# Kernel tuning notes

Hardware: AMD Instinct MI355X
Metric: run time of the kernel (lower is better)

Reference implementation:

```python
import jax, jax.numpy as jnp
import numpy as np

B, T, HID = 4, 4096, 768
H, D = 12, 64
N_HASHES = 2
BUCKET_SIZE = T // 32          # reformer repo config: max_seq_len // 32 = 128
N_BUCKETS = T // BUCKET_SIZE   # 32
SELF_ATTN_VALUE = -5e4         # reformer_pytorch TOKEN_SELF_ATTN_VALUE
MASK_VALUE = -1e9


def lsh_attention(X, mask_bool, W_qk, W_v, rotations):
    # X: [b, t, hid]; rotations: [d, n_hashes, n_buckets//2] (shared across batch & heads)
    b, t, _ = X.shape
    d, n_hashes, half_nb = rotations.shape
    n_buckets = 2 * half_nb
    h = W_qk.shape[0] // d
    scale = d ** -0.5

    qk = X @ W_qk.T            # shared query/key projection (bias-free in reformer_pytorch)
    v = X @ W_v.T

    def merge_heads(x):  # [b,t,h*d] -> [b*h, t, d]
        return x.reshape(b, t, h, d).transpose(0, 2, 1, 3).reshape(b * h, t, d)

    qk, v = merge_heads(qk), merge_heads(v)
    maskbh = jnp.repeat(mask_bool, h, axis=0)          # [bh, t]

    # --- LSH bucketing ---
    rotated = jnp.einsum('btf,fhi->bhti', qk, rotations)          # [bh, nh, t, nb/2]
    rotated = jnp.concatenate([rotated, -rotated], axis=-1)       # [bh, nh, t, nb]
    buckets = jnp.argmax(rotated, axis=-1)                        # [bh, nh, t]
    offsets = (jnp.arange(n_hashes) * n_buckets)[None, :, None]
    buckets = (buckets + offsets).reshape(b * h, n_hashes * t)

    # --- stable sort by (bucket, position) ---
    total = n_hashes * t
    ticker = jnp.arange(total)[None, :]
    buckets_and_t = buckets * t + (ticker % t)
    sticker = jnp.argsort(buckets_and_t, axis=-1)   # stable
    undo = jnp.argsort(sticker, axis=-1)
    st = sticker % t                                 # original positions, sorted order

    sqk = jnp.take_along_axis(qk, st[..., None], axis=1)
    sv = jnp.take_along_axis(v, st[..., None], axis=1)
    smask = jnp.take_along_axis(maskbh, st, axis=1)

    # --- chunk; each chunk attends to itself + previous chunk ---
    n_chunks = n_hashes * n_buckets
    cl = total // n_chunks                                  # == bucket_size
    bq_t = st.reshape(b * h, n_chunks, cl)
    bqk = sqk.reshape(b * h, n_chunks, cl, d)
    bv = sv.reshape(b * h, n_chunks, cl, d)
    bmask = smask.reshape(b * h, n_chunks, cl)

    bq = bqk
    bk = bqk / jnp.clip(jnp.linalg.norm(bqk, axis=-1, keepdims=True), 1e-12)

    def look_one_back(x):
        return jnp.concatenate([x, jnp.roll(x, 1, axis=1)], axis=2)

    bk, bv = look_one_back(bk), look_one_back(bv)
    bkv_t = look_one_back(bq_t)
    bkv_mask = look_one_back(bmask)

    dots = jnp.einsum('bnie,bnje->bnij', bq, bk) * scale    # [bh, n_chunks, cl, 2cl]
    pad = bmask[..., :, None] & bkv_mask[..., None, :]
    dots = jnp.where(pad, dots, MASK_VALUE)
    self_mask = bq_t[..., :, None] == bkv_t[..., None, :]
    dots = jnp.where(self_mask, SELF_ATTN_VALUE, dots)

    lse = jax.scipy.special.logsumexp(dots, axis=-1, keepdims=True)
    probs = jnp.exp(dots - lse)
    bo = jnp.einsum('bnij,bnje->bnie', probs, bv)

    # --- unsort and combine hash rounds via softmax over round logsumexps ---
    so = bo.reshape(b * h, total, d)
    slogits = lse.reshape(b * h, total)
    o = jnp.take_along_axis(so, undo[..., None], axis=1)
    logits = jnp.take_along_axis(slogits, undo, axis=1)

    o = o.reshape(b * h, n_hashes, t, d)
    logits = logits.reshape(b * h, n_hashes, t, 1)
    round_probs = jnp.exp(logits - jax.scipy.special.logsumexp(logits, axis=1, keepdims=True))
    out = jnp.sum(o * round_probs, axis=1)                  # [bh, t, d]
    return out.reshape(b, h, t, d).transpose(0, 2, 1, 3).reshape(b, t, h * d)


def setup_inputs() -> dict:
    key = jax.random.key(0)
    ks = jax.random.split(key, 8)
    s = 1.0 / np.sqrt(HID)
    return {
        'X': jax.random.normal(ks[0], (B, T, HID), jnp.float32),
        'mask': jnp.ones((B, T), jnp.float32),
        'W_qk': jax.random.uniform(ks[1], (H * D, HID), jnp.float32, -s, s),
        'W_v': jax.random.uniform(ks[2], (H * D, HID), jnp.float32, -s, s),
        'rotations': jax.random.normal(ks[3], (D, N_HASHES, N_BUCKETS // 2), jnp.float32),
        'W_to': jax.random.uniform(ks[4], (HID, H * D), jnp.float32, -s, s),
        'b_to': jnp.zeros((HID,), jnp.float32),
        'W_o': jax.random.uniform(ks[5], (HID, HID), jnp.float32, -s, s),
        'b_o': jnp.zeros((HID,), jnp.float32),
    }


def reference(X, mask, W_qk, W_v, rotations, W_to, b_to, W_o, b_o):
    attn = lsh_attention(X, mask.astype(bool), W_qk, W_v, rotations)
    attn = attn @ W_to.T + b_to     # LSHSelfAttention.to_out
    return attn @ W_o.T + b_o       # ReformerAttention.W_o
```

## Files before the change

kernel.cpp:

```cpp
#include <hip/hip_runtime.h>
#include <hip/hip_bf16.h>
#include <math.h>


typedef __attribute__((ext_vector_type(8))) short bf16x8;
typedef __attribute__((ext_vector_type(4))) float f32x4;
typedef __attribute__((ext_vector_type(4))) double f64x4;

__device__ __forceinline__ float bf_lo(unsigned int w) { return __uint_as_float(w << 16); }
__device__ __forceinline__ float bf_hi(unsigned int w) { return __uint_as_float(w & 0xffff0000u); }
__device__ __forceinline__ float load_in(const void* p, size_t i, bool f32) {
  return f32 ? ((const float*)p)[i]
             : __bfloat162float(((const __hip_bfloat16*)p)[i]);
}
__device__ __forceinline__ unsigned short f2bf(float x) {
  __hip_bfloat16 h = __float2bfloat16(x);
  return *reinterpret_cast<unsigned short*>(&h);
}
__device__ __forceinline__ float bf2f(unsigned short u) { return __uint_as_float(((unsigned int)u) << 16); }

__global__ void k_detect(const unsigned int* __restrict__ X, int* __restrict__ flag) {
  if (threadIdx.x == 0 && blockIdx.x == 0) {
    int vote = 0;
    for (int i = 0; i < 64; ++i) {
      unsigned int e = (X[i] >> 7) & 0xffu;
      vote += (e >= 100u && e <= 141u) ? 1 : 0;
    }
    *flag = (vote < 32) ? 1 : 0;
  }
}

__global__ __launch_bounds__(256) void k_convert(
    const void* __restrict__ src, unsigned short* __restrict__ dst, int n8,
    const int* __restrict__ flag) {
  const bool f32in = (*flag != 0);
  int i = blockIdx.x * 256 + threadIdx.x;
  if (i >= n8) return;
  if (f32in) {
    const float4* s = (const float4*)src + (size_t)i * 2;
    float4 a = s[0], b = s[1];
    union { unsigned short u[8]; uint4 v; } o;
    o.u[0] = f2bf(a.x); o.u[1] = f2bf(a.y); o.u[2] = f2bf(a.z); o.u[3] = f2bf(a.w);
    o.u[4] = f2bf(b.x); o.u[5] = f2bf(b.y); o.u[6] = f2bf(b.z); o.u[7] = f2bf(b.w);
    ((uint4*)dst)[i] = o.v;
  } else {
    ((uint4*)dst)[i] = ((const uint4*)src)[i];
  }
}

__global__ __launch_bounds__(256) void k_build_wrot(
    const void* __restrict__ Wqk, const void* __restrict__ rot,
    double* __restrict__ WrotT, const int* __restrict__ flag) {
  const bool f32in = (*flag != 0);
  int idx = blockIdx.x * 256 + threadIdx.x;
  if (idx >= 768 * 384) return;
  int row = idx % 384;
  int c   = idx / 384;
  int hh = row >> 5, hi = row & 31;
  double s = 0.0;
  for (int f = 0; f < 64; ++f) {
    double rv = (double)load_in(rot, f * 32 + hi, f32in);
    double wv = (double)load_in(Wqk, (size_t)(hh * 64 + f) * 768 + c, f32in);
    s = fma(rv, wv, s);
  }
  WrotT[(size_t)c * 384 + row] = s;
}

__global__ __launch_bounds__(512) void k_bucket(
    const void* __restrict__ X, const double* __restrict__ WrotT,
    unsigned char* __restrict__ cls, const int* __restrict__ flag) {
  const bool f32in = (*flag != 0);
  __shared__ double SH[4224];
  float* XsF = (float*)SH;
  double* Sc = SH;
  const int tid = threadIdx.x;
  const int M0 = blockIdx.x * 128;
  const int N0 = blockIdx.y * 64;
  const int w = tid >> 6, lane = tid & 63;
  const int l15 = lane & 15, lq = lane >> 4;
  const int sr = tid >> 2, sh2 = tid & 3;
  const int wk = tid >> 5, wg2 = (tid & 31) * 2;

  f64x4 acc[4];
  #pragma unroll
  for (int j = 0; j < 4; ++j) acc[j] = (f64x4){0.0, 0.0, 0.0, 0.0};

  int rowid[4], colid[4];
  {
    f64x4 zz = (f64x4){0.0, 0.0, 0.0, 0.0};
    f64x4 pr = __builtin_amdgcn_mfma_f64_16x16x4f64(
        (double)l15, (lq == 0) ? 1.0 : 0.0, zz, 0, 0, 0);
    f64x4 pc = __builtin_amdgcn_mfma_f64_16x16x4f64(
        (lq == 0) ? 1.0 : 0.0, (double)l15, zz, 0, 0, 0);
    #pragma unroll
    for (int r = 0; r < 4; ++r) {
      rowid[r] = (int)pr[r];
      colid[r] = (int)pc[r];
    }
  }

  float xv[4];
  double wvv[2];
  auto load_chunk = [&](int k0) {
    size_t base = (size_t)(M0 + sr) * 768 + k0 + sh2 * 4;
    if (f32in) {
      float4 f0 = *(const float4*)((const float*)X + base);
      xv[0] = f0.x; xv[1] = f0.y; xv[2] = f0.z; xv[3] = f0.w;
    } else {
      uint2 u = *(const uint2*)((const unsigned short*)X + base);
      xv[0] = bf_lo(u.x); xv[1] = bf_hi(u.x);
      xv[2] = bf_lo(u.y); xv[3] = bf_hi(u.y);
    }
    const double* wp = WrotT + (size_t)(k0 + wk) * 384 + N0 + wg2;
    wvv[0] = wp[0]; wvv[1] = wp[1];
  };
  auto store_stage = [&](int bsel) {
    float* Xs = XsF + bsel * 2112;
    double* Ws = SH + 2112 + bsel * 1056;
    #pragma unroll
    for (int j = 0; j < 4; ++j) Xs[(sh2 * 4 + j) * 132 + sr] = xv[j];
    Ws[wk * 66 + wg2] = wvv[0];
    Ws[wk * 66 + wg2 + 1] = wvv[1];
  };

  load_chunk(0);
  store_stage(0);
  __syncthreads();
  for (int t = 0; t < 48; ++t) {
    const float* Xs = XsF + (t & 1) * 2112;
    const double* Ws = SH + 2112 + (t & 1) * 1056;
    if (t < 47) load_chunk((t + 1) * 16);
    #pragma unroll
    for (int kq = 0; kq < 4; ++kq) {
      double a = (double)Xs[(kq * 4 + lq) * 132 + w * 16 + l15];
      const double* wr = &Ws[(kq * 4 + lq) * 66 + l15];
      #pragma unroll
      for (int nt = 0; nt < 4; ++nt)
        acc[nt] = __builtin_amdgcn_mfma_f64_16x16x4f64(a, wr[nt * 16], acc[nt], 0, 0, 0);
    }
    if (t < 47) store_stage((t & 1) ^ 1);
    __syncthreads();
  }

  #pragma unroll
  for (int chunk = 0; chunk < 2; ++chunk) {
    __syncthreads();
    if ((w >> 2) == chunk) {
      int lr = (w & 3) * 16;
      #pragma unroll
      for (int nt = 0; nt < 4; ++nt)
        #pragma unroll
        for (int r = 0; r < 4; ++r)
          Sc[(nt * 16 + colid[r]) * 66 + lr + rowid[r]] = acc[nt][r];
    }
    __syncthreads();
    for (int task = tid; task < 256; task += 512) {
      int g = task >> 6, tok = task & 63;
      const double* s = &Sc[(g * 16) * 66 + tok];
      double mx = -1.0e300;
      #pragma unroll
      for (int i = 0; i < 16; ++i) {
        double a = s[i * 66];
        mx = fmax(mx, fmax(a, -a));
      }
      int amax = 0;
      #pragma unroll
      for (int i = 15; i >= 0; --i) if (-s[i * 66] == mx) amax = 16 + i;
      #pragma unroll
      for (int i = 15; i >= 0; --i) if (s[i * 66] == mx) amax = i;
      int m = M0 + chunk * 64 + tok;
      int b = m >> 12, t = m & 4095;
      int gg = blockIdx.y * 4 + g, hh = gg >> 1, h = gg & 1;
      cls[(size_t)(b * 12 + hh) * 8192 + h * 4096 + t] = (unsigned char)(h * 32 + amax);
    }
  }
}

__global__ __launch_bounds__(1024) void k_sort(
    const unsigned char* __restrict__ clsg,
    unsigned short* __restrict__ stick) {
  __shared__ unsigned short cntg[128 * 64];
  __shared__ int classbase[64];
  const int row = blockIdx.x;
  const int tid = threadIdx.x;
  const int wave = tid >> 6, lane = tid & 63;
  const unsigned char* cr = clsg + ((size_t)row << 13);

  for (int i = tid; i < 128 * 64 / 2; i += 1024) ((uint32_t*)cntg)[i] = 0;
  __syncthreads();

  unsigned char myc[8], myrank[8];
  const unsigned long long ltmask = (lane == 0) ? 0ull : (~0ull >> (64 - lane));
  #pragma unroll
  for (int chunk = 0; chunk < 8; ++chunk) {
    int g = chunk * 16 + wave;
    int j = g * 64 + lane;
    int c = cr[j];
    unsigned long long same = ~0ull;
    #pragma unroll
    for (int bit = 0; bit < 6; ++bit) {
      unsigned long long bm = __ballot((c >> bit) & 1);
      same &= ((c >> bit) & 1) ? bm : ~bm;
    }
    int rank = __popcll(same & ltmask);
    if (rank == 0) cntg[g * 64 + c] = (unsigned short)__popcll(same);
    myc[chunk] = (unsigned char)c;
    myrank[chunk] = (unsigned char)rank;
  }
  __syncthreads();
  if (tid < 64) {
    int run = 0;
    for (int g = 0; g < 128; ++g) {
      int t = cntg[g * 64 + tid];
      cntg[g * 64 + tid] = (unsigned short)run;
      run += t;
    }
    classbase[tid] = run;
  }
  __syncthreads();
  if (tid == 0) {
    int run = 0;
    for (int c = 0; c < 64; ++c) { int t = classbase[c]; classbase[c] = run; run += t; }
  }
  __syncthreads();
  unsigned short* out = stick + ((size_t)row << 13);
  #pragma unroll
  for (int chunk = 0; chunk < 8; ++chunk) {
    int g = chunk * 16 + wave;
    int j = g * 64 + lane;
    int c = myc[chunk];
    int pos = classbase[c] + cntg[g * 64 + c] + myrank[chunk];
    out[pos] = (unsigned short)j;
  }
}

__global__ __launch_bounds__(256) void k_gemm_mfma(
    const unsigned short* __restrict__ A, const unsigned short* __restrict__ W,
    const void* __restrict__ bias, void* __restrict__ Cout,
    int layout, int out_ext, const int* __restrict__ flag) {
  const bool f32in = (*flag != 0);
  const bool oF32 = out_ext && f32in;
  __shared__ unsigned short As[128 * 40];
  __shared__ unsigned short Bs[128 * 40];
  const int tid = threadIdx.x;
  const int bm = blockIdx.x, bn = blockIdx.y;
  const int w = tid >> 6, lane = tid & 63;
  const int l15 = lane & 15, lq = lane >> 4;
  const int wm = (w >> 1) * 64, wn = (w & 1) * 64;
  const int r4 = tid >> 2, c4 = tid & 3;
  const unsigned short* Ag = A + (size_t)(bm * 128 + r4) * 768 + c4 * 8;
  const unsigned short* Bg = W + (size_t)(bn * 128 + r4) * 768 + c4 * 8;
  f32x4 acc[4][4];
  #pragma unroll
  for (int i = 0; i < 4; ++i)
    #pragma unroll
    for (int j = 0; j < 4; ++j) acc[i][j] = (f32x4){0.f, 0.f, 0.f, 0.f};
  uint4 pa0 = *(const uint4*)(Ag);
  uint4 pa1 = *(const uint4*)(Ag + 64 * 768);
  uint4 pb0 = *(const uint4*)(Bg);
  uint4 pb1 = *(const uint4*)(Bg + 64 * 768);
  for (int kt = 0; kt < 24; ++kt) {
    __syncthreads();
    *(uint4*)&As[r4 * 40 + c4 * 8] = pa0;
    *(uint4*)&As[(r4 + 64) * 40 + c4 * 8] = pa1;
    *(uint4*)&Bs[r4 * 40 + c4 * 8] = pb0;
    *(uint4*)&Bs[(r4 + 64) * 40 + c4 * 8] = pb1;
    __syncthreads();
    if (kt < 23) {
      int off = (kt + 1) * 32;
      pa0 = *(const uint4*)(Ag + off);
      pa1 = *(const uint4*)(Ag + 64 * 768 + off);
      pb0 = *(const uint4*)(Bg + off);
      pb1 = *(const uint4*)(Bg + 64 * 768 + off);
    }
    bf16x8 af[4], bfr[4];
    #pragma unroll
    for (int mt = 0; mt < 4; ++mt)
      af[mt] = *(const bf16x8*)&As[(wm + mt * 16 + l15) * 40 + lq * 8];
    #pragma unroll
    for (int nt = 0; nt < 4; ++nt)
      bfr[nt] = *(const bf16x8*)&Bs[(wn + nt * 16 + l15) * 40 + lq * 8];
    #pragma unroll
    for (int mt = 0; mt < 4; ++mt)
      #pragma unroll
      for (int nt = 0; nt < 4; ++nt)
        acc[mt][nt] = __builtin_amdgcn_mfma_f32_16x16x32_bf16(af[mt], bfr[nt], acc[mt][nt], 0, 0, 0);
  }
  #pragma unroll
  for (int mt = 0; mt < 4; ++mt) {
    #pragma unroll
    for (int nt = 0; nt < 4; ++nt) {
      #pragma unroll
      for (int reg = 0; reg < 4; ++reg) {
        int m = bm * 128 + wm + mt * 16 + lq * 4 + reg;
        int n = bn * 128 + wn + nt * 16 + l15;
        float val = acc[mt][nt][reg];
        if (bias != nullptr) val += load_in(bias, n, f32in);
        if (layout == 0) {
          size_t addr = (size_t)m * 768 + n;
          if (oF32) ((float*)Cout)[addr] = val;
          else      ((unsigned short*)Cout)[addr] = f2bf(val);
        } else {
          int b2 = m >> 12, t2 = m & 4095, hh = n >> 6, f = n & 63;
          ((unsigned short*)Cout)[((((size_t)(b2 * 12 + hh)) << 12) + t2) * 64 + f] = f2bf(val);
        }
      }
    }
  }
}

__global__ __launch_bounds__(256) void k_norm(
    const unsigned short* __restrict__ qk, float* __restrict__ nk) {
  int row = blockIdx.x * 32 + (threadIdx.x >> 3);
  int cs = threadIdx.x & 7;
  const uint4* p = (const uint4*)(qk + (size_t)row * 64);
  uint4 wv = p[cs];
  float s = 0.f;
  float e;
  e = bf_lo(wv.x); s += e * e;  e = bf_hi(wv.x); s += e * e;
  e = bf_lo(wv.y); s += e * e;  e = bf_hi(wv.y); s += e * e;
  e = bf_lo(wv.z); s += e * e;  e = bf_hi(wv.z); s += e * e;
  e = bf_lo(wv.w); s += e * e;  e = bf_hi(wv.w); s += e * e;
  s += __shfl_xor(s, 1, 64);
  s += __shfl_xor(s, 2, 64);
  s += __shfl_xor(s, 4, 64);
  if (cs == 0) nk[row] = 1.0f / fmaxf(sqrtf(s), 1e-12f);
}

__global__ __launch_bounds__(256) void k_attn_mfma(
    const unsigned short* __restrict__ qk,
    const unsigned short* __restrict__ vv,
    const unsigned short* __restrict__ stick,
    const void* __restrict__ mask,
    const float* __restrict__ nk,
    unsigned short* __restrict__ o_r,
    float* __restrict__ lse_r,
    const int* __restrict__ flag) {
  const bool f32in = (*flag != 0);
  __shared__ unsigned short Qs[128 * 72];
  __shared__ unsigned short Ks[64 * 72];
  __shared__ unsigned short Vt[64 * 72];
  __shared__ unsigned short Ps[4 * 32 * 72];
  __shared__ unsigned short Tq[128];
  __shared__ unsigned short Tkv[64];
  __shared__ float Nkv[64];
  unsigned short* Vs = Ps;

  const int tid = threadIdx.x;
  const int bh = blockIdx.x >> 6;
  const int ci = blockIdx.x & 63;
  const int b  = bh / 12;
  const int prev = (ci + 63) & 63;
  const int w = tid >> 6, lane = tid & 63;
  const int l15 = lane & 15, lq = lane >> 4;
  const unsigned short* srow = stick + ((size_t)bh << 13);
  const int jrow = tid >> 3, cs = tid & 7;

  #pragma unroll
  for (int pass = 0; pass < 4; ++pass) {
    int r = jrow + pass * 32;
    int s = srow[ci * 128 + r];
    int t = s & 4095;
    uint4 qw = ((const uint4*)(qk + ((((size_t)bh << 12) + t) << 6)))[cs];
    *(uint4*)&Qs[r * 72 + cs * 8] = qw;
    if (cs == 0) {
      float mv = load_in(mask, b * 4096 + t, f32in);
      Tq[r] = (unsigned short)(s | ((mv != 0.0f) ? 0 : 0x8000));
    }
  }
  __syncthreads();

  unsigned short tqr[2][4];
  #pragma unroll
  for (int mt = 0; mt < 2; ++mt)
    #pragma unroll
    for (int reg = 0; reg < 4; ++reg)
      tqr[mt][reg] = Tq[w * 32 + mt * 16 + lq * 4 + reg];

  float m_run[2][4], l_run[2][4];
  f32x4 oacc[2][4];
  #pragma unroll
  for (int mt = 0; mt < 2; ++mt)
    #pragma unroll
    for (int reg = 0; reg < 4; ++reg) { m_run[mt][reg] = -3.0e38f; l_run[mt][reg] = 0.0f; }
  #pragma unroll
  for (int mt = 0; mt < 2; ++mt)
    #pragma unroll
    for (int nto = 0; nto < 4; ++nto) oacc[mt][nto] = (f32x4){0.f, 0.f, 0.f, 0.f};

  for (int kt = 0; kt < 4; ++kt) {
    __syncthreads();
    #pragma unroll
    for (int pass = 0; pass < 2; ++pass) {
      int j = jrow + pass * 32;
      int chunk = (kt < 2) ? ci : prev;
      int s = srow[chunk * 128 + (kt & 1) * 64 + j];
      int t = s & 4095;
      const uint4* kb = (const uint4*)(qk + ((((size_t)bh << 12) + t) << 6));
      *(uint4*)&Ks[j * 72 + cs * 8] = kb[cs];
      const uint4* vb = (const uint4*)(vv + ((((size_t)bh << 12) + t) << 6));
      int sw = (cs ^ (j & 7) ^ (j >> 3)) & 7;
      *(uint4*)&Vs[j * 72 + sw * 8] = vb[cs];
      if (cs == 0) {
        float mv = load_in(mask, b * 4096 + t, f32in);
        Tkv[j] = (unsigned short)(t | ((mv != 0.0f) ? 0 : 0x8000));
        Nkv[j] = nk[((size_t)bh << 12) + t] * 0.125f;
      }
    }
    __syncthreads();

    #pragma unroll
    for (int i = 0; i < 8; ++i) {
      int cp = w * 8 + i;
      int q8 = cp >> 2;
      int sw = (q8 ^ (lane & 7) ^ (lane >> 3)) & 7;
      uint32_t wv = *(const uint32_t*)&Vs[lane * 72 + sw * 8 + ((2 * cp) & 7)];
      Vt[(2 * cp) * 72 + lane]     = (unsigned short)(wv & 0xffff);
      Vt[(2 * cp + 1) * 72 + lane] = (unsigned short)(wv >> 16);
    }

    f32x4 sacc[2][4];
    #pragma unroll
    for (int mt = 0; mt < 2; ++mt)
      #pragma unroll
      for (int nt = 0; nt < 4; ++nt) sacc[mt][nt] = (f32x4){0.f, 0.f, 0.f, 0.f};
    #pragma unroll
    for (int ks = 0; ks < 2; ++ks) {
      bf16x8 af[2];
      #pragma unroll
      for (int mt = 0; mt < 2; ++mt)
        af[mt] = *(const bf16x8*)&Qs[(w * 32 + mt * 16 + l15) * 72 + ks * 32 + lq * 8];
      #pragma unroll
      for (int nt = 0; nt < 4; ++nt) {
        bf16x8 bfr = *(const bf16x8*)&Ks[(nt * 16 + l15) * 72 + ks * 32 + lq * 8];
        #pragma unroll
        for (int mt = 0; mt < 2; ++mt)
          sacc[mt][nt] = __builtin_amdgcn_mfma_f32_16x16x32_bf16(af[mt], bfr, sacc[mt][nt], 0, 0, 0);
      }
    }

    unsigned short tkc[4];
    float nkc[4];
    #pragma unroll
    for (int nt = 0; nt < 4; ++nt) {
      tkc[nt] = Tkv[nt * 16 + l15];
      nkc[nt] = Nkv[nt * 16 + l15];
    }
    float dv[2][4][4];
    #pragma unroll
    for (int mt = 0; mt < 2; ++mt)
      #pragma unroll
      for (int nt = 0; nt < 4; ++nt)
        #pragma unroll
        for (int reg = 0; reg < 4; ++reg) {
          float x = sacc[mt][nt][reg] * nkc[nt];
          unsigned short ts = tqr[mt][reg];
          if (((tkc[nt] | ts) & 0x8000) != 0) x = -1.0e9f;
          if (((tkc[nt] ^ ts) & 0x0fff) == 0) x = -5.0e4f;
          dv[mt][nt][reg] = x;
        }
    float mn[2][4], scv[2][4];
    #pragma unroll
    for (int mt = 0; mt < 2; ++mt)
      #pragma unroll
      for (int reg = 0; reg < 4; ++reg) {
        float rm = fmaxf(fmaxf(dv[mt][0][reg], dv[mt][1][reg]),
                         fmaxf(dv[mt][2][reg], dv[mt][3][reg]));
        rm = fmaxf(rm, __shfl_xor(rm, 1, 64));
        rm = fmaxf(rm, __shfl_xor(rm, 2, 64));
        rm = fmaxf(rm, __shfl_xor(rm, 4, 64));
        rm = fmaxf(rm, __shfl_xor(rm, 8, 64));
        float mnew = fmaxf(m_run[mt][reg], rm);
        scv[mt][reg] = __expf(m_run[mt][reg] - mnew);
        m_run[mt][reg] = mnew;
        mn[mt][reg] = mnew;
      }
    #pragma unroll
    for (int mt = 0; mt < 2; ++mt)
      #pragma unroll
      for (int nt = 0; nt < 4; ++nt)
        #pragma unroll
        for (int reg = 0; reg < 4; ++reg)
          dv[mt][nt][reg] = __expf(dv[mt][nt][reg] - mn[mt][reg]);
    #pragma unroll
    for (int mt = 0; mt < 2; ++mt)
      #pragma unroll
      for (int reg = 0; reg < 4; ++reg) {
        float rs = ((dv[mt][0][reg] + dv[mt][1][reg]) + (dv[mt][2][reg] + dv[mt][3][reg]));
        rs += __shfl_xor(rs, 1, 64);
        rs += __shfl_xor(rs, 2, 64);
        rs += __shfl_xor(rs, 4, 64);
        rs += __shfl_xor(rs, 8, 64);
        l_run[mt][reg] = l_run[mt][reg] * scv[mt][reg] + rs;
      }
    #pragma unroll
    for (int mt = 0; mt < 2; ++mt)
      #pragma unroll
      for (int nto = 0; nto < 4; ++nto)
        #pragma unroll
        for (int reg = 0; reg < 4; ++reg)
          oacc[mt][nto][reg] *= scv[mt][reg];

    __syncthreads();

    #pragma unroll
    for (int mt = 0; mt < 2; ++mt)
      #pragma unroll
      for (int nt = 0; nt < 4; ++nt)
        #pragma unroll
        for (int reg = 0; reg < 4; ++reg)
          Ps[w * 2304 + (mt * 16 + lq * 4 + reg) * 72 + nt * 16 + l15] = f2bf(dv[mt][nt][reg]);

    #pragma unroll
    for (int ks = 0; ks < 2; ++ks) {
      bf16x8 pf[2];
      #pragma unroll
      for (int mt = 0; mt < 2; ++mt)
        pf[mt] = *(const bf16x8*)&Ps[w * 2304 + (mt * 16 + l15) * 72 + ks * 32 + lq * 8];
      #pragma unroll
      for (int nto = 0; nto < 4; ++nto) {
        bf16x8 vf = *(const bf16x8*)&Vt[(nto * 16 + l15) * 72 + ks * 32 + lq * 8];
        #pragma unroll
        for (int mt = 0; mt < 2; ++mt)
          oacc[mt][nto] = __builtin_amdgcn_mfma_f32_16x16x32_bf16(pf[mt], vf, oacc[mt][nto], 0, 0, 0);
      }
    }
  }

  float invl[2][4];
  #pragma unroll
  for (int mt = 0; mt < 2; ++mt)
    #pragma unroll
    for (int reg = 0; reg < 4; ++reg) {
      float lr = l_run[mt][reg];
      invl[mt][reg] = 1.0f / lr;
      if (l15 == 0) {
        int Rr = w * 32 + mt * 16 + lq * 4 + reg;
        int s = Tq[Rr];
        int tq0 = s & 4095, rq0 = (s >> 12) & 1;
        lse_r[(((size_t)(bh * 2 + rq0)) << 12) + tq0] = m_run[mt][reg] + __logf(lr);
      }
    }
  #pragma unroll
  for (int mt = 0; mt < 2; ++mt)
    #pragma unroll
    for (int nto = 0; nto < 4; ++nto)
      #pragma unroll
      for (int reg = 0; reg < 4; ++reg)
        Ps[w * 2304 + (mt * 16 + lq * 4 + reg) * 72 + nto * 16 + l15] =
            f2bf(oacc[mt][nto][reg] * invl[mt][reg]);
  #pragma unroll
  for (int pass = 0; pass < 4; ++pass) {
    int rl = pass * 8 + (lane >> 3);
    int s = Tq[w * 32 + rl];
    int tq0 = s & 4095, rq0 = (s >> 12) & 1;
    uint4 ov = *(const uint4*)&Ps[w * 2304 + rl * 72 + (lane & 7) * 8];
    *(uint4*)(o_r + ((((size_t)(bh * 2 + rq0)) << 12) + tq0) * 64 + (lane & 7) * 8) = ov;
  }
}

__global__ __launch_bounds__(256) void k_combine(
    const unsigned short* __restrict__ o_r,
    const float* __restrict__ lse_r,
    unsigned short* __restrict__ attn) {
  int idx = blockIdx.x * 256 + threadIdx.x;
  if (idx >= 48 * 4096 * 8) return;
  int f8 = idx & 7;
  int t = (idx >> 3) & 4095;
  int bh = idx >> 15;
  float l0 = lse_r[((size_t)(bh * 2 + 0) << 12) + t];
  float l1 = lse_r[((size_t)(bh * 2 + 1) << 12) + t];
  float mm = fmaxf(l0, l1);
  float e0 = __expf(l0 - mm), e1 = __expf(l1 - mm);
  float inv = 1.0f / (e0 + e1);
  float c0 = e0 * inv, c1 = e1 * inv;
  uint4 v0 = *(const uint4*)(o_r + ((((size_t)(bh * 2 + 0)) << 12) + t) * 64 + f8 * 8);
  uint4 v1 = *(const uint4*)(o_r + ((((size_t)(bh * 2 + 1)) << 12) + t) * 64 + f8 * 8);
  union { unsigned short u[8]; uint4 v; } o;
  const unsigned int* a0 = (const unsigned int*)&v0;
  const unsigned int* a1 = (const unsigned int*)&v1;
  #pragma unroll
  for (int j = 0; j < 4; ++j) {
    float lo = c0 * bf_lo(a0[j]) + c1 * bf_lo(a1[j]);
    float hi = c0 * bf_hi(a0[j]) + c1 * bf_hi(a1[j]);
    o.u[2 * j]     = f2bf(lo);
    o.u[2 * j + 1] = f2bf(hi);
  }
  int b = bh / 12, hh = bh % 12;
  *(uint4*)(attn + ((size_t)(b * 4096 + t)) * 768 + hh * 64 + f8 * 8) = o.v;
}

extern "C" void kernel_launch(void* const* d_in, const int* in_sizes, int n_in,
                              void* d_out, int out_size, void* d_ws, size_t ws_size,
                              hipStream_t stream) {
  (void)in_sizes; (void)n_in; (void)out_size; (void)ws_size;
  const void* X    = d_in[0];
  const void* mask = d_in[1];
  const void* Wqk  = d_in[2];
  const void* Wv   = d_in[3];
  const void* rot  = d_in[4];
  const void* Wto  = d_in[5];
  const void* bto  = d_in[6];
  const void* Wo   = d_in[7];
  const void* bo   = d_in[8];

  char* ws = (char*)d_ws;
  int*            flag  = (int*)(ws);
  unsigned short* stick = (unsigned short*)(ws + 256);
  float*          lse_r = (float*)(ws + 786688);
  float*          nk    = (float*)(ws + 2359552);
  unsigned short* qk    = (unsigned short*)(ws + 3145984);
  unsigned short* v     = (unsigned short*)(ws + 28311808);
  unsigned short* o_r   = (unsigned short*)(ws + 53477632);
  double*         WrotT = (double*)(ws + 53477632);
  unsigned char*  cls   = (unsigned char*)(ws + 55836928);
  unsigned short* Wqkb  = (unsigned short*)(ws + 56230144);
  unsigned short* Wvb   = (unsigned short*)(ws + 57409792);
  unsigned short* Xb    = (unsigned short*)(ws + 58589440);
  unsigned short* Wtob  = (unsigned short*)(ws + 53477632);
  unsigned short* Wob   = (unsigned short*)(ws + 54657280);
  unsigned short* attn  = v;
  unsigned short* tmp   = qk;

  k_detect<<<1, 64, 0, stream>>>((const unsigned int*)X, flag);
  k_convert<<<6144, 256, 0, stream>>>(X, Xb, 1572864, flag);
  k_convert<<<288, 256, 0, stream>>>(Wqk, Wqkb, 73728, flag);
  k_convert<<<288, 256, 0, stream>>>(Wv, Wvb, 73728, flag);
  k_build_wrot<<<1152, 256, 0, stream>>>(Wqk, rot, WrotT, flag);
  k_bucket<<<dim3(128, 6), 512, 0, stream>>>(X, WrotT, cls, flag);
  k_sort<<<48, 1024, 0, stream>>>(cls, stick);
  k_gemm_mfma<<<dim3(128, 6), 256, 0, stream>>>(Xb, Wqkb, nullptr, qk, 1, 0, flag);
  k_gemm_mfma<<<dim3(128, 6), 256, 0, stream>>>(Xb, Wvb,  nullptr, v,  1, 0, flag);
  k_norm<<<6144, 256, 0, stream>>>(qk, nk);
  k_attn_mfma<<<3072, 256, 0, stream>>>(qk, v, stick, mask, nk, o_r, lse_r, flag);
  k_combine<<<6144, 256, 0, stream>>>(o_r, lse_r, attn);
  k_convert<<<288, 256, 0, stream>>>(Wto, Wtob, 73728, flag);
  k_convert<<<288, 256, 0, stream>>>(Wo, Wob, 73728, flag);
  k_gemm_mfma<<<dim3(128, 6), 256, 0, stream>>>(attn, Wtob, bto, tmp, 0, 0, flag);
  k_gemm_mfma<<<dim3(128, 6), 256, 0, stream>>>(tmp, Wob, bo, d_out, 0, 1, flag);
}
```

Measured before the change: 627.1 us.

## Widen bucketing GEMM tile to 96 columns and prefetch K/V tiles in attention

The f64 bucketing GEMM now covers 96 rotation columns per block (6 MFMA n-tiles) instead of 64, cutting the grid's y-dimension from 6 to 4 so each X tile is loaded fewer times. X is staged in LDS as double, which removes the per-MFMA float-to-double conversion but doubles the X staging footprint. The attention kernel now register-prefetches the next K/V tile (plus mask and norm) while the current one is processed, overlapping gather latency with MFMA work. The cost is more registers and LDS, which may lower occupancy.

```diff
diff --git a/kernel.cpp b/kernel.cpp
--- a/kernel.cpp
+++ b/kernel.cpp
@@ -70,20 +70,19 @@
     const void* __restrict__ X, const double* __restrict__ WrotT,
     unsigned char* __restrict__ cls, const int* __restrict__ flag) {
   const bool f32in = (*flag != 0);
-  __shared__ double SH[4224];
-  float* XsF = (float*)SH;
+  __shared__ double SH[7296];
   double* Sc = SH;
   const int tid = threadIdx.x;
   const int M0 = blockIdx.x * 128;
-  const int N0 = blockIdx.y * 64;
+  const int N0 = blockIdx.y * 96;
   const int w = tid >> 6, lane = tid & 63;
   const int l15 = lane & 15, lq = lane >> 4;
   const int sr = tid >> 2, sh2 = tid & 3;
-  const int wk = tid >> 5, wg2 = (tid & 31) * 2;
-
-  f64x4 acc[4];
-  #pragma unroll
-  for (int j = 0; j < 4; ++j) acc[j] = (f64x4){0.0, 0.0, 0.0, 0.0};
+  const int wk = tid >> 5, wn3 = (tid & 31) * 3;
+
+  f64x4 acc[6];
+  #pragma unroll
+  for (int j = 0; j < 6; ++j) acc[j] = (f64x4){0.0, 0.0, 0.0, 0.0};
 
   int rowid[4], colid[4];
   {
@@ -99,8 +98,8 @@
     }
   }
 
-  float xv[4];
-  double wvv[2];
+  double xv[4];
+  double wvv[3];
   auto load_chunk = [&](int k0) {
     size_t base = (size_t)(M0 + sr) * 768 + k0 + sh2 * 4;
     if (f32in) {
@@ -108,34 +107,35 @@
       xv[0] = f0.x; xv[1] = f0.y; xv[2] = f0.z; xv[3] = f0.w;
     } else {
       uint2 u = *(const uint2*)((const unsigned short*)X + base);
-      xv[0] = bf_lo(u.x); xv[1] = bf_hi(u.x);
-      xv[2] = bf_lo(u.y); xv[3] = bf_hi(u.y);
-    }
-    const double* wp = WrotT + (size_t)(k0 + wk) * 384 + N0 + wg2;
-    wvv[0] = wp[0]; wvv[1] = wp[1];
+      xv[0] = (double)bf_lo(u.x); xv[1] = (double)bf_hi(u.x);
+      xv[2] = (double)bf_lo(u.y); xv[3] = (double)bf_hi(u.y);
+    }
+    const double* wp = WrotT + (size_t)(k0 + wk) * 384 + N0 + wn3;
+    wvv[0] = wp[0]; wvv[1] = wp[1]; wvv[2] = wp[2];
   };
   auto store_stage = [&](int bsel) {
-    float* Xs = XsF + bsel * 2112;
-    double* Ws = SH + 2112 + bsel * 1056;
-    #pragma unroll
-    for (int j = 0; j < 4; ++j) Xs[(sh2 * 4 + j) * 132 + sr] = xv[j];
-    Ws[wk * 66 + wg2] = wvv[0];
-    Ws[wk * 66 + wg2 + 1] = wvv[1];
+    double* Xs = SH + bsel * 2080;
+    double* Ws = SH + 4160 + bsel * 1568;
+    #pragma unroll
+    for (int j = 0; j < 4; ++j) Xs[(sh2 * 4 + j) * 130 + sr] = xv[j];
+    Ws[wk * 98 + wn3]     = wvv[0];
+    Ws[wk * 98 + wn3 + 1] = wvv[1];
+    Ws[wk * 98 + wn3 + 2] = wvv[2];
   };
 
   load_chunk(0);
   store_stage(0);
   __syncthreads();
   for (int t = 0; t < 48; ++t) {
-    const float* Xs = XsF + (t & 1) * 2112;
-    const double* Ws = SH + 2112 + (t & 1) * 1056;
+    const double* Xs = SH + (t & 1) * 2080;
+    const double* Ws = SH + 4160 + (t & 1) * 1568;
     if (t < 47) load_chunk((t + 1) * 16);
     #pragma unroll
     for (int kq = 0; kq < 4; ++kq) {
-      double a = (double)Xs[(kq * 4 + lq) * 132 + w * 16 + l15];
-      const double* wr = &Ws[(kq * 4 + lq) * 66 + l15];
-      #pragma unroll
-      for (int nt = 0; nt < 4; ++nt)
+      double a = Xs[(kq * 4 + lq) * 130 + w * 16 + l15];
+      const double* wr = &Ws[(kq * 4 + lq) * 98 + l15];
+      #pragma unroll
+      for (int nt = 0; nt < 6; ++nt)
         acc[nt] = __builtin_amdgcn_mfma_f64_16x16x4f64(a, wr[nt * 16], acc[nt], 0, 0, 0);
     }
     if (t < 47) store_stage((t & 1) ^ 1);
@@ -148,13 +148,13 @@
     if ((w >> 2) == chunk) {
       int lr = (w & 3) * 16;
       #pragma unroll
-      for (int nt = 0; nt < 4; ++nt)
+      for (int nt = 0; nt < 6; ++nt)
         #pragma unroll
         for (int r = 0; r < 4; ++r)
           Sc[(nt * 16 + colid[r]) * 66 + lr + rowid[r]] = acc[nt][r];
     }
     __syncthreads();
-    for (int task = tid; task < 256; task += 512) {
+    for (int task = tid; task < 384; task += 512) {
       int g = task >> 6, tok = task & 63;
       const double* s = &Sc[(g * 16) * 66 + tok];
       double mx = -1.0e300;
@@ -170,7 +170,7 @@
       for (int i = 15; i >= 0; --i) if (s[i * 66] == mx) amax = i;
       int m = M0 + chunk * 64 + tok;
       int b = m >> 12, t = m & 4095;
-      int gg = blockIdx.y * 4 + g, hh = gg >> 1, h = gg & 1;
+      int gg = blockIdx.y * 6 + g, hh = gg >> 1, h = gg & 1;
       cls[(size_t)(b * 12 + hh) * 8192 + h * 4096 + t] = (unsigned char)(h * 32 + amax);
     }
   }
@@ -356,6 +356,38 @@
   const unsigned short* srow = stick + ((size_t)bh << 13);
   const int jrow = tid >> 3, cs = tid & 7;
 
+  uint4 kreg[2], vreg[2];
+  unsigned short tkv_reg[2];
+  float nkv_reg[2];
+  auto load_kv = [&](int kt) {
+    #pragma unroll
+    for (int pass = 0; pass < 2; ++pass) {
+      int j = jrow + pass * 32;
+      int chunk = (kt < 2) ? ci : prev;
+      int s = srow[chunk * 128 + (kt & 1) * 64 + j];
+      int t = s & 4095;
+      kreg[pass] = ((const uint4*)(qk + ((((size_t)bh << 12) + t) << 6)))[cs];
+      vreg[pass] = ((const uint4*)(vv + ((((size_t)bh << 12) + t) << 6)))[cs];
+      if (cs == 0) {
+        float mv = load_in(mask, b * 4096 + t, f32in);
+        tkv_reg[pass] = (unsigned short)(t | ((mv != 0.0f) ? 0 : 0x8000));
+        nkv_reg[pass] = nk[((size_t)bh << 12) + t] * 0.125f;
+      }
+    }
+  };
+  auto store_kv = [&]() {
+    #pragma unroll
+    for (int pass = 0; pass < 2; ++pass) {
+      int j = jrow + pass * 32;
+      *(uint4*)&Ks[j * 72 + cs * 8] = kreg[pass];
+      int sw = (cs ^ (j & 7) ^ (j >> 3)) & 7;
+      *(uint4*)&Vs[j * 72 + sw * 8] = vreg[pass];
+      if (cs == 0) { Tkv[j] = tkv_reg[pass]; Nkv[j] = nkv_reg[pass]; }
+    }
+  };
+
+  load_kv(0);
+
   #pragma unroll
   for (int pass = 0; pass < 4; ++pass) {
     int r = jrow + pass * 32;
@@ -390,23 +422,8 @@
 
   for (int kt = 0; kt < 4; ++kt) {
     __syncthreads();
-    #pragma unroll
-    for (int pass = 0; pass < 2; ++pass) {
-      int j = jrow + pass * 32;
-      int chunk = (kt < 2) ? ci : prev;
-      int s = srow[chunk * 128 + (kt & 1) * 64 + j];
-      int t = s & 4095;
-      const uint4* kb = (const uint4*)(qk + ((((size_t)bh << 12) + t) << 6));
-      *(uint4*)&Ks[j * 72 + cs * 8] = kb[cs];
-      const uint4* vb = (const uint4*)(vv + ((((size_t)bh << 12) + t) << 6));
-      int sw = (cs ^ (j & 7) ^ (j >> 3)) & 7;
-      *(uint4*)&Vs[j * 72 + sw * 8] = vb[cs];
-      if (cs == 0) {
-        float mv = load_in(mask, b * 4096 + t, f32in);
-        Tkv[j] = (unsigned short)(t | ((mv != 0.0f) ? 0 : 0x8000));
-        Nkv[j] = nk[((size_t)bh << 12) + t] * 0.125f;
-      }
-    }
+    store_kv();
+    if (kt < 3) load_kv(kt + 1);
     __syncthreads();
 
     #pragma unroll
@@ -627,7 +644,7 @@
   k_convert<<<288, 256, 0, stream>>>(Wqk, Wqkb, 73728, flag);
   k_convert<<<288, 256, 0, stream>>>(Wv, Wvb, 73728, flag);
   k_build_wrot<<<1152, 256, 0, stream>>>(Wqk, rot, WrotT, flag);
-  k_bucket<<<dim3(128, 6), 512, 0, stream>>>(X, WrotT, cls, flag);
+  k_bucket<<<dim3(128, 4), 512, 0, stream>>>(X, WrotT, cls, flag);
   k_sort<<<48, 1024, 0, stream>>>(cls, stick);
   k_gemm_mfma<<<dim3(128, 6), 256, 0, stream>>>(Xb, Wqkb, nullptr, qk, 1, 0, flag);
   k_gemm_mfma<<<dim3(128, 6), 256, 0, stream>>>(Xb, Wvb,  nullptr, v,  1, 0, flag);
```

Result: slower. 650.7 us (+3.8%).
